# Kernel tuning notes

Measured on AMD Instinct MI355X. Metric: run time of the kernel, lower is better.

The kernel has to match this reference:

```python
import jax, jax.numpy as jnp
import numpy as np

KH = KW = 3
K = KH * KW
STRIDE = 1
PAD = 1
DIL = 1
GROUPS = 1
DG = 1  # deformable_groups
CIN = 256
COUT = 256
DC = 64  # depth_channels


def conv2d(x, w, b):
    out = jax.lax.conv_general_dilated(
        x, w, (STRIDE, STRIDE), [(PAD, PAD), (PAD, PAD)],
        rhs_dilation=(DIL, DIL), dimension_numbers=('NCHW', 'OIHW', 'NCHW'))
    return out + b[None, :, None, None]


def deform_sample(x, offset, mask):
    """Modulated deformable im2col. x:[N,C,H,W], offset:[N,DG*2*K,Ho,Wo],
    mask:[N,DG*K,Ho,Wo] or None. Returns cols [N,C,K,Ho,Wo]."""
    N, C, H, W = x.shape
    Ho = (H + 2 * PAD - (DIL * (KH - 1) + 1)) // STRIDE + 1
    Wo = (W + 2 * PAD - (DIL * (KW - 1) + 1)) // STRIDE + 1
    ky, kx = jnp.meshgrid(jnp.arange(KH), jnp.arange(KW), indexing='ij')
    # base sampling grid per kernel tap: [K,Ho,Wo]
    base_y = (jnp.arange(Ho) * STRIDE - PAD)[None, :, None] + (ky.reshape(-1) * DIL)[:, None, None]
    base_x = (jnp.arange(Wo) * STRIDE - PAD)[None, None, :] + (kx.reshape(-1) * DIL)[:, None, None]
    off = offset.reshape(N, DG, K, 2, Ho, Wo)  # [...,0]=dy, [...,1]=dx (CUDA layout)
    y = base_y[None, None].astype(x.dtype) + off[:, :, :, 0]
    xx = base_x[None, None].astype(x.dtype) + off[:, :, :, 1]
    y0 = jnp.floor(y)
    x0 = jnp.floor(xx)
    ly = y - y0
    lx = xx - x0
    y0i = y0.astype(jnp.int32)
    x0i = x0.astype(jnp.int32)
    xg = x.reshape(N, DG, C // DG, H * W)

    def gather(iy, ix):
        valid = ((iy >= 0) & (iy < H) & (ix >= 0) & (ix < W)).astype(x.dtype)
        idx = (jnp.clip(iy, 0, H - 1) * W + jnp.clip(ix, 0, W - 1)).reshape(N, DG, 1, K * Ho * Wo)
        v = jnp.take_along_axis(xg, idx, axis=3).reshape(N, DG, C // DG, K, Ho, Wo)
        return v * valid[:, :, None]

    v00 = gather(y0i, x0i)
    v01 = gather(y0i, x0i + 1)
    v10 = gather(y0i + 1, x0i)
    v11 = gather(y0i + 1, x0i + 1)
    w00 = (1 - ly) * (1 - lx)
    w01 = (1 - ly) * lx
    w10 = ly * (1 - lx)
    w11 = ly * lx
    cols = (v00 * w00[:, :, None] + v01 * w01[:, :, None]
            + v10 * w10[:, :, None] + v11 * w11[:, :, None])
    if mask is not None:
        cols = cols * mask.reshape(N, DG, 1, K, Ho, Wo)
    return cols.reshape(N, C, K, Ho, Wo)


def deform_conv2d(x, offset, mask, weight, bias):
    cols = deform_sample(x, offset, mask)  # [N,C,K,Ho,Wo]
    N, C, _, Ho, Wo = cols.shape
    Cout = weight.shape[0]
    cg = C // GROUPS
    cols = cols.reshape(N, GROUPS, cg * K, Ho * Wo)
    wg = weight.reshape(GROUPS, Cout // GROUPS, cg * K)
    out = jnp.einsum('gok,ngkp->ngop', wg, cols).reshape(N, Cout, Ho, Wo)
    return out + bias[None, :, None, None]


def setup_inputs() -> dict:
    key = jax.random.key(0)
    ks = jax.random.split(key, 8)
    x = jax.random.normal(ks[0], (4, CIN, 64, 64), dtype=jnp.float32)
    depth = jax.random.normal(ks[1], (4, DC, 64, 64), dtype=jnp.float32)
    stdv = 1.0 / np.sqrt(CIN * KH * KW)
    weight = jax.random.uniform(ks[2], (COUT, CIN // GROUPS, KH, KW), minval=-stdv, maxval=stdv, dtype=jnp.float32)
    bias = jnp.zeros((COUT,), jnp.float32)
    # offset/mask convs are zero-init in the module; use small random weights
    # so the irregular gather path is actually exercised.
    off_w = 0.05 * jax.random.normal(ks[3], (DG * 2 * K, CIN + DC, KH, KW), dtype=jnp.float32)
    off_b = 0.05 * jax.random.normal(ks[4], (DG * 2 * K,), dtype=jnp.float32)
    mask_w = 0.05 * jax.random.normal(ks[5], (DG * K, DC, KH, KW), dtype=jnp.float32)
    mask_b = 0.05 * jax.random.normal(ks[6], (DG * K,), dtype=jnp.float32)
    return {"x": x, "depth": depth, "weight": weight, "bias": bias,
            "off_w": off_w, "off_b": off_b, "mask_w": mask_w, "mask_b": mask_b}


def reference(x, depth, weight, bias, off_w, off_b, mask_w, mask_b):
    # offset = conv_offset(cat(x, depth))
    offset = conv2d(jnp.concatenate([x, depth], axis=1), off_w, off_b)
    # mask = sigmoid(DeformConv(depth, offset))  (non-modulated deform conv)
    mask = jax.nn.sigmoid(deform_conv2d(depth, offset, None, mask_w, mask_b))
    # modulated deformable conv on x
    return deform_conv2d(x, offset, mask, weight, bias)
```

## Files before the change

kernel.cpp:

```cpp
#include <hip/hip_runtime.h>


typedef __bf16 bf16x8 __attribute__((ext_vector_type(8)));
typedef float f32x4 __attribute__((ext_vector_type(4)));
typedef float float2_u __attribute__((ext_vector_type(2), aligned(4)));

__device__ __forceinline__ unsigned short f2bf(float f) {
  unsigned b = __float_as_uint(f);
  return (unsigned short)((b + 0x7fffu + ((b >> 16) & 1u)) >> 16);
}

__global__ __launch_bounds__(256) void k_prep_weight(
    const float* __restrict__ w, unsigned short* __restrict__ wbf)
{
  const int i = blockIdx.x * 256 + threadIdx.x;
  wbf[i] = f2bf(w[i]);
}

__global__ __launch_bounds__(256) void k_offset_conv(
    const float* __restrict__ x, const float* __restrict__ depth,
    const float* __restrict__ off_w, const float* __restrict__ off_b,
    float* __restrict__ offs)
{
  const int seg = blockIdx.x >> 8;
  const int nh  = blockIdx.x & 255;
  const int n = nh >> 6, ho = nh & 63;
  const int tid = threadIdx.x;
  const int lane = tid & 63;
  const int wave = tid >> 6;

  float acc[18];
#pragma unroll
  for (int i = 0; i < 18; ++i) acc[i] = 0.f;

  const int c0 = __builtin_amdgcn_readfirstlane(seg * 80 + wave * 20);

  for (int ci = 0; ci < 20; ++ci) {
    const int c = c0 + ci;
    const float* p = (c < 256) ? (x + (((n << 8) + c) << 12))
                               : (depth + (((n << 6) + (c - 256)) << 12));
    const float v0 = (ho > 0)  ? p[((ho - 1) << 6) + lane] : 0.f;
    const float v1 =             p[( ho      << 6) + lane];
    const float v2 = (ho < 63) ? p[((ho + 1) << 6) + lane] : 0.f;

    float v[9];
#pragma unroll
    for (int ky = 0; ky < 3; ++ky) {
      const float r = (ky == 0) ? v0 : ((ky == 1) ? v1 : v2);
#pragma unroll
      for (int kx = 0; kx < 3; ++kx) {
        const int src = lane + kx - 1;
        const float s = __shfl(r, src & 63);
        v[ky * 3 + kx] = (src >= 0 && src < 64) ? s : 0.f;
      }
    }
    const float* wp = off_w + c * 9;
#pragma unroll
    for (int co = 0; co < 18; ++co) {
      const float* w = wp + co * 2880;
#pragma unroll
      for (int t = 0; t < 9; ++t) acc[co] += v[t] * w[t];
    }
  }

  __shared__ float red[4][18][64];
#pragma unroll
  for (int co = 0; co < 18; ++co) red[wave][co][lane] = acc[co];
  __syncthreads();
  for (int o = tid; o < 18 * 64; o += 256) {
    const int co = o >> 6, wo = o & 63;
    float s = red[0][co][wo] + red[1][co][wo] + red[2][co][wo] + red[3][co][wo];
    if (seg == 0) s += off_b[co];
    atomicAdd(&offs[((n * 18 + co) << 12) + (ho << 6) + wo], s);
  }
}

__global__ __launch_bounds__(512) void k_mask_conv(
    const float* __restrict__ depth, const float* __restrict__ offs,
    const float* __restrict__ mask_w, const float* __restrict__ mask_b,
    float* __restrict__ mask)
{
  const int n  = blockIdx.x >> 6;
  const int ho = blockIdx.x & 63;
  const int tid  = threadIdx.x;
  const int lane = tid & 63;
  const int wave = tid >> 6;
  const int wo = lane;

  int i00[9], i01[9], i10[9], i11[9];
  float cw00[9], cw01[9], cw10[9], cw11[9];
  const float* op = offs + ((n * 18) << 12) + (ho << 6) + wo;
#pragma unroll
  for (int k = 0; k < 9; ++k) {
    const float dy = op[(2 * k) << 12];
    const float dx = op[(2 * k + 1) << 12];
    const float yy = (float)(ho - 1 + k / 3) + dy;
    const float xx = (float)(wo - 1 + k % 3) + dx;
    const float y0f = floorf(yy), x0f = floorf(xx);
    const float ly = yy - y0f, lx = xx - x0f;
    const int y0 = (int)y0f, x0 = (int)x0f;
    const int y0c = min(max(y0, 0), 63),     x0c = min(max(x0, 0), 63);
    const int y1c = min(max(y0 + 1, 0), 63), x1c = min(max(x0 + 1, 0), 63);
    const float fy0 = (y0 >= 0 && y0 < 64) ? 1.f : 0.f;
    const float fy1 = (y0 >= -1 && y0 < 63) ? 1.f : 0.f;
    const float fx0 = (x0 >= 0 && x0 < 64) ? 1.f : 0.f;
    const float fx1 = (x0 >= -1 && x0 < 63) ? 1.f : 0.f;
    i00[k] = (y0c << 6) + x0c;  i01[k] = (y0c << 6) + x1c;
    i10[k] = (y1c << 6) + x0c;  i11[k] = (y1c << 6) + x1c;
    cw00[k] = (1.f - ly) * (1.f - lx) * fy0 * fx0;
    cw01[k] = (1.f - ly) * lx * fy0 * fx1;
    cw10[k] = ly * (1.f - lx) * fy1 * fx0;
    cw11[k] = ly * lx * fy1 * fx1;
  }

  float acc[9];
#pragma unroll
  for (int i = 0; i < 9; ++i) acc[i] = 0.f;

  const int cbase = __builtin_amdgcn_readfirstlane(wave * 8);
  for (int cc = 0; cc < 8; ++cc) {
    const int c = cbase + cc;
    const float* p = depth + (((n << 6) + c) << 12);
    float val[9];
#pragma unroll
    for (int k = 0; k < 9; ++k) {
      val[k] = p[i00[k]] * cw00[k] + p[i01[k]] * cw01[k] +
               p[i10[k]] * cw10[k] + p[i11[k]] * cw11[k];
    }
    const float* wp = mask_w + c * 9;
#pragma unroll
    for (int co = 0; co < 9; ++co) {
#pragma unroll
      for (int k = 0; k < 9; ++k) acc[co] += val[k] * wp[co * 576 + k];
    }
  }

  __shared__ float red[8][9][64];
#pragma unroll
  for (int co = 0; co < 9; ++co) red[wave][co][lane] = acc[co];
  __syncthreads();
  for (int o = tid; o < 9 * 64; o += 512) {
    const int co = o >> 6, w2 = o & 63;
    float s = mask_b[co];
#pragma unroll
    for (int w = 0; w < 8; ++w) s += red[w][co][w2];
    mask[((n * 9 + co) << 12) + (ho << 6) + w2] = 1.f / (1.f + expf(-s));
  }
}

__global__ __launch_bounds__(512, 2) void k_deform_gemm(
    const float* __restrict__ x, const float* __restrict__ offs,
    const float* __restrict__ mask, const unsigned short* __restrict__ wbf,
    const float* __restrict__ bias, float* __restrict__ out)
{
  __shared__ __align__(16) unsigned short Bs[2][64][72];
  __shared__ float4 pwT[9][64];
  __shared__ int2   piT[9][64];

  const int tid = threadIdx.x;
  const int b    = blockIdx.x;
  const int xcd  = b & 7, slot = b >> 3;
  const int n    = xcd >> 1;
  const int ho0  = ((xcd & 1) << 5) + slot;
  const int pxb  = ho0 << 6;
  const int pxg0 = (n << 12) + pxb;

  for (int e = tid; e < 576; e += 512) {
    const int tap = e >> 6, pl = e & 63;
    const int pxg = pxg0 + pl;
    const int wo = pl;
    const float dy = offs[((n * 18 + 2 * tap) << 12) + pxb + pl];
    const float dx = offs[((n * 18 + 2 * tap + 1) << 12) + pxb + pl];
    const float m  = mask[((n * 9 + tap) << 12) + pxb + pl];
    (void)pxg;
    const float yy = (float)(ho0 - 1 + tap / 3) + dy;
    const float xx = (float)(wo - 1 + tap % 3) + dx;
    const float y0f = floorf(yy), x0f = floorf(xx);
    const float ly = yy - y0f, lx = xx - x0f;
    const int y0 = (int)y0f, x0 = (int)x0f;
    const int y0c = min(max(y0, 0), 63);
    const int y1c = min(max(y0 + 1, 0), 63);
    const float fy0 = (y0 >= 0 && y0 < 64) ? 1.f : 0.f;
    const float fy1 = (y0 >= -1 && y0 < 63) ? 1.f : 0.f;
    const int x0c = min(max(x0, 0), 63);
    const int x1c = min(max(x0 + 1, 0), 63);
    const int bx  = min(max(x0, 0), 62);
    const float vx0 = (x0 >= 0 && x0 < 64) ? 1.f : 0.f;
    const float vx1 = (x0 >= -1 && x0 < 63) ? 1.f : 0.f;
    const float wl = (1.f - lx) * vx0 * ((x0c == bx) ? 1.f : 0.f)
                   + lx * vx1 * ((x1c == bx) ? 1.f : 0.f);
    const float wr = (1.f - lx) * vx0 * ((x0c == bx + 1) ? 1.f : 0.f)
                   + lx * vx1 * ((x1c == bx + 1) ? 1.f : 0.f);
    const float a0 = (1.f - ly) * fy0 * m;
    const float a1 = ly * fy1 * m;
    pwT[tap][pl] = make_float4(wl * a0, wr * a0, wl * a1, wr * a1);
    piT[tap][pl] = make_int2((((y0c << 6) + bx) << 2), (((y1c << 6) + bx) << 2));
  }
  __syncthreads();

  const int pxl = tid & 63;
  const int oct = tid >> 6;
  const float* xn = x + ((long)(n << 8) << 12);

  auto sample = [&](int kc, int buf) {
    const int kk0 = kc + (oct << 3);
    int c = (int)(((unsigned)kk0 * 7282u) >> 16);
    int tap = kk0 - 9 * c;
    const char* p = (const char*)(xn + (c << 12));
    __align__(16) unsigned short v[8];
#pragma unroll
    for (int j = 0; j < 8; ++j) {
      const float4 w = pwT[tap][pxl];
      const int2 ii  = piT[tap][pxl];
      const float2_u pa = *(const float2_u*)(p + ii.x);
      const float2_u pb = *(const float2_u*)(p + ii.y);
      v[j] = f2bf(pa.x * w.x + pa.y * w.y + pb.x * w.z + pb.y * w.w);
      if (++tap == 9) { tap = 0; p += 16384; }
    }
    *(int4*)&Bs[buf][pxl][oct << 3] = *(const int4*)v;
  };

  f32x4 acc[2][4];
#pragma unroll
  for (int mt = 0; mt < 2; ++mt)
#pragma unroll
    for (int nt = 0; nt < 4; ++nt)
#pragma unroll
      for (int r = 0; r < 4; ++r) acc[mt][nt][r] = 0.f;

  sample(0, 0);
  __syncthreads();

  const int wv   = oct;
  const int lane = tid & 63;
  const int mrow = lane & 15;
  const int koct = lane >> 4;

  for (int ic = 0; ic < 36; ++ic) {
    const int kc = ic << 6;
    bf16x8 af[2][2];
#pragma unroll
    for (int mt = 0; mt < 2; ++mt)
#pragma unroll
      for (int ks = 0; ks < 2; ++ks) {
        const int row = (wv << 5) + (mt << 4) + mrow;
        const int col = kc + (ks << 5) + (koct << 3);
        af[mt][ks] = *(const bf16x8*)(wbf + row * 2304 + col);
      }

    if (ic + 1 < 36) sample((ic + 1) << 6, (ic + 1) & 1);

    const int buf = ic & 1;
#pragma unroll
    for (int ks = 0; ks < 2; ++ks)
#pragma unroll
      for (int nt = 0; nt < 4; ++nt) {
        const bf16x8 bfr =
            *(const bf16x8*)&Bs[buf][(nt << 4) + mrow][(ks << 5) + (koct << 3)];
        acc[0][nt] = __builtin_amdgcn_mfma_f32_16x16x32_bf16(af[0][ks], bfr,
                                                             acc[0][nt], 0, 0, 0);
        acc[1][nt] = __builtin_amdgcn_mfma_f32_16x16x32_bf16(af[1][ks], bfr,
                                                             acc[1][nt], 0, 0, 0);
      }
    __syncthreads();
  }

#pragma unroll
  for (int mt = 0; mt < 2; ++mt)
#pragma unroll
    for (int nt = 0; nt < 4; ++nt)
#pragma unroll
      for (int r = 0; r < 4; ++r) {
        const int co = (wv << 5) + (mt << 4) + ((lane >> 4) << 2) + r;
        const int pxg = pxb + (nt << 4) + (lane & 15);
        out[(((n << 8) + co) << 12) + pxg] = acc[mt][nt][r] + bias[co];
      }
}

extern "C" void kernel_launch(void* const* d_in, const int* in_sizes, int n_in,
                              void* d_out, int out_size, void* d_ws, size_t ws_size,
                              hipStream_t stream) {
  const float* x      = (const float*)d_in[0];
  const float* depth  = (const float*)d_in[1];
  const float* weight = (const float*)d_in[2];
  const float* bias   = (const float*)d_in[3];
  const float* off_w  = (const float*)d_in[4];
  const float* off_b  = (const float*)d_in[5];
  const float* mask_w = (const float*)d_in[6];
  const float* mask_b = (const float*)d_in[7];
  float* out = (float*)d_out;

  float* offs = (float*)d_ws;
  float* mask = offs + 294912;
  unsigned short* wbf = (unsigned short*)(mask + 147456);

  hipMemsetAsync(offs, 0, 294912 * sizeof(float), stream);
  k_prep_weight<<<2304, 256, 0, stream>>>(weight, wbf);
  k_offset_conv<<<1024, 256, 0, stream>>>(x, depth, off_w, off_b, offs);
  k_mask_conv<<<256, 512, 0, stream>>>(depth, offs, mask_w, mask_b, mask);
  k_deform_gemm<<<256, 512, 0, stream>>>(x, offs, mask, wbf, bias, out);
}
```

Measured before the change: 281.2 us.

## Halve deform GEMM pixel tile and split gather into issue/finish around MFMAs

The deform GEMM tile shrinks from 64 to 32 pixels per block, so 512 blocks launch instead of 256, with launch bounds raised to allow four blocks per CU. The bilinear sampling is split into an issue phase that starts the global gathers before the MFMA loop and a finish phase that blends and stores to LDS after it, hiding gather latency behind the matrix math. The aim is more parallelism across the 256 CUs and better latency hiding. The cost is that each block reuses the weight fragments over only half as many pixels, doubling weight reads, and the 4-blocks-per-CU bound may force tighter register allocation.

```diff
diff --git a/kernel.cpp b/kernel.cpp
--- a/kernel.cpp
+++ b/kernel.cpp
@@ -148,32 +148,30 @@
   }
 }
 
-__global__ __launch_bounds__(512, 2) void k_deform_gemm(
+__global__ __launch_bounds__(512, 4) void k_deform_gemm(
     const float* __restrict__ x, const float* __restrict__ offs,
     const float* __restrict__ mask, const unsigned short* __restrict__ wbf,
     const float* __restrict__ bias, float* __restrict__ out)
 {
-  __shared__ __align__(16) unsigned short Bs[2][64][72];
-  __shared__ float4 pwT[9][64];
-  __shared__ int2   piT[9][64];
+  __shared__ __align__(16) unsigned short Bs[2][32][72];
+  __shared__ float4 pwT[9][32];
+  __shared__ int2   piT[9][32];
 
   const int tid = threadIdx.x;
   const int b    = blockIdx.x;
   const int xcd  = b & 7, slot = b >> 3;
   const int n    = xcd >> 1;
-  const int ho0  = ((xcd & 1) << 5) + slot;
-  const int pxb  = ho0 << 6;
-  const int pxg0 = (n << 12) + pxb;
-
-  for (int e = tid; e < 576; e += 512) {
-    const int tap = e >> 6, pl = e & 63;
-    const int pxg = pxg0 + pl;
-    const int wo = pl;
-    const float dy = offs[((n * 18 + 2 * tap) << 12) + pxb + pl];
-    const float dx = offs[((n * 18 + 2 * tap + 1) << 12) + pxb + pl];
-    const float m  = mask[((n * 9 + tap) << 12) + pxb + pl];
-    (void)pxg;
-    const float yy = (float)(ho0 - 1 + tap / 3) + dy;
+  const int ho   = ((xcd & 1) << 5) + (slot >> 1);
+  const int wo0  = (slot & 1) << 5;
+  const int pxb  = (ho << 6) + wo0;
+
+  if (tid < 288) {
+    const int tap = tid >> 5, pl = tid & 31;
+    const int wo = wo0 + pl;
+    const float dy = offs[((n * 18 + 2 * tap) << 12) + (ho << 6) + wo];
+    const float dx = offs[((n * 18 + 2 * tap + 1) << 12) + (ho << 6) + wo];
+    const float m  = mask[((n * 9 + tap) << 12) + (ho << 6) + wo];
+    const float yy = (float)(ho - 1 + tap / 3) + dy;
     const float xx = (float)(wo - 1 + tap % 3) + dx;
     const float y0f = floorf(yy), x0f = floorf(xx);
     const float ly = yy - y0f, lx = xx - x0f;
@@ -198,43 +196,57 @@
   }
   __syncthreads();
 
-  const int pxl = tid & 63;
-  const int oct = tid >> 6;
-  const float* xn = x + ((long)(n << 8) << 12);
-
-  auto sample = [&](int kc, int buf) {
-    const int kk0 = kc + (oct << 3);
-    int c = (int)(((unsigned)kk0 * 7282u) >> 16);
-    int tap = kk0 - 9 * c;
-    const char* p = (const char*)(xn + (c << 12));
-    __align__(16) unsigned short v[8];
-#pragma unroll
-    for (int j = 0; j < 8; ++j) {
-      const float4 w = pwT[tap][pxl];
-      const int2 ii  = piT[tap][pxl];
-      const float2_u pa = *(const float2_u*)(p + ii.x);
-      const float2_u pb = *(const float2_u*)(p + ii.y);
-      v[j] = f2bf(pa.x * w.x + pa.y * w.y + pb.x * w.z + pb.y * w.w);
-      if (++tap == 9) { tap = 0; p += 16384; }
-    }
-    *(int4*)&Bs[buf][pxl][oct << 3] = *(const int4*)v;
-  };
-
-  f32x4 acc[2][4];
-#pragma unroll
-  for (int mt = 0; mt < 2; ++mt)
-#pragma unroll
-    for (int nt = 0; nt < 4; ++nt)
-#pragma unroll
-      for (int r = 0; r < 4; ++r) acc[mt][nt][r] = 0.f;
-
-  sample(0, 0);
-  __syncthreads();
-
-  const int wv   = oct;
+  const int pxl  = tid & 31;
+  const int kq   = tid >> 5;
+  const int wv   = tid >> 6;
   const int lane = tid & 63;
   const int mrow = lane & 15;
   const int koct = lane >> 4;
+  const float* xn = x + ((long)(n << 8) << 12);
+
+  float4   w_[4];
+  float2_u pa_[4], pb_[4];
+
+  auto issue = [&](int kc) {
+    const int k0 = kc + (kq << 2);
+    int c = (int)(((unsigned)k0 * 7282u) >> 16);
+    int tt = k0 - 9 * c;
+    int2 ii[4];
+    const char* pp[4];
+    const char* p = (const char*)(xn + (c << 12));
+#pragma unroll
+    for (int j = 0; j < 4; ++j) {
+      w_[j] = pwT[tt][pxl];
+      ii[j] = piT[tt][pxl];
+      pp[j] = p;
+      if (++tt == 9) { tt = 0; p += 16384; }
+    }
+#pragma unroll
+    for (int j = 0; j < 4; ++j) {
+      pa_[j] = *(const float2_u*)(pp[j] + ii[j].x);
+      pb_[j] = *(const float2_u*)(pp[j] + ii[j].y);
+    }
+  };
+  auto finish = [&](int buf) {
+    __align__(8) unsigned short v[4];
+#pragma unroll
+    for (int j = 0; j < 4; ++j)
+      v[j] = f2bf(pa_[j].x * w_[j].x + pa_[j].y * w_[j].y +
+                  pb_[j].x * w_[j].z + pb_[j].y * w_[j].w);
+    *(int2*)&Bs[buf][pxl][kq << 2] = *(const int2*)v;
+  };
+
+  f32x4 acc[2][2];
+#pragma unroll
+  for (int mt = 0; mt < 2; ++mt)
+#pragma unroll
+    for (int nt = 0; nt < 2; ++nt)
+#pragma unroll
+      for (int r = 0; r < 4; ++r) acc[mt][nt][r] = 0.f;
+
+  issue(0);
+  finish(0);
+  __syncthreads();
 
   for (int ic = 0; ic < 36; ++ic) {
     const int kc = ic << 6;
@@ -248,13 +260,13 @@
         af[mt][ks] = *(const bf16x8*)(wbf + row * 2304 + col);
       }
 
-    if (ic + 1 < 36) sample((ic + 1) << 6, (ic + 1) & 1);
+    if (ic + 1 < 36) issue((ic + 1) << 6);
 
     const int buf = ic & 1;
 #pragma unroll
     for (int ks = 0; ks < 2; ++ks)
 #pragma unroll
-      for (int nt = 0; nt < 4; ++nt) {
+      for (int nt = 0; nt < 2; ++nt) {
         const bf16x8 bfr =
             *(const bf16x8*)&Bs[buf][(nt << 4) + mrow][(ks << 5) + (koct << 3)];
         acc[0][nt] = __builtin_amdgcn_mfma_f32_16x16x32_bf16(af[0][ks], bfr,
@@ -262,13 +274,15 @@
         acc[1][nt] = __builtin_amdgcn_mfma_f32_16x16x32_bf16(af[1][ks], bfr,
                                                              acc[1][nt], 0, 0, 0);
       }
+
+    if (ic + 1 < 36) finish((ic + 1) & 1);
     __syncthreads();
   }
 
 #pragma unroll
   for (int mt = 0; mt < 2; ++mt)
 #pragma unroll
-    for (int nt = 0; nt < 4; ++nt)
+    for (int nt = 0; nt < 2; ++nt)
 #pragma unroll
       for (int r = 0; r < 4; ++r) {
         const int co = (wv << 5) + (mt << 4) + ((lane >> 4) << 2) + r;
@@ -298,5 +312,5 @@
   k_prep_weight<<<2304, 256, 0, stream>>>(weight, wbf);
   k_offset_conv<<<1024, 256, 0, stream>>>(x, depth, off_w, off_b, offs);
   k_mask_conv<<<256, 512, 0, stream>>>(depth, offs, mask_w, mask_b, mask);
-  k_deform_gemm<<<256, 512, 0, stream>>>(x, offs, mask, wbf, bias, out);
-}
+  k_deform_gemm<<<512, 512, 0, stream>>>(x, offs, mask, wbf, bias, out);
+}
```

New measurement: 301.0 us. 7.0% more time.

## Stage input row strips in LDS via async global-to-LDS loads for bilinear gather

Applied to the files above, without the earlier changes.

The deform GEMM kernel now asynchronously copies an 18-row strip of each input channel into a 9-slot LDS ring using global_load_lds, and bilinear samples read from LDS when the row falls in the strip, falling back to global memory otherwise. The B tile goes from double-buffered to single-buffered, and the gather now runs after the MFMA stage with an extra barrier, so sampling and MMA no longer overlap. Index packing is compressed to one int. The aim is to replace scattered global gathers with LDS reads, at the cost of less compute overlap, more LDS use that may lower occupancy, and a possible race on the ring slots if the async copies are not waited on before they are read.

```diff
diff --git a/kernel.cpp b/kernel.cpp
--- a/kernel.cpp
+++ b/kernel.cpp
@@ -148,32 +148,46 @@
   }
 }
 
+__device__ __forceinline__ void stage_channel(const float* src, float* dstb,
+                                              int lane) {
+  const char* s = (const char*)src + lane * 16;
+  char* d = (char*)dstb;
+#pragma unroll
+  for (int j = 0; j < 4; ++j)
+    __builtin_amdgcn_global_load_lds(
+        (const __attribute__((address_space(1))) void*)(s + j * 1024),
+        (__attribute__((address_space(3))) void*)(d + j * 1024), 16, 0, 0);
+  if (lane < 32)
+    __builtin_amdgcn_global_load_lds(
+        (const __attribute__((address_space(1))) void*)(s + 4096),
+        (__attribute__((address_space(3))) void*)(d + 4096), 16, 0, 0);
+}
+
 __global__ __launch_bounds__(512, 2) void k_deform_gemm(
     const float* __restrict__ x, const float* __restrict__ offs,
     const float* __restrict__ mask, const unsigned short* __restrict__ wbf,
     const float* __restrict__ bias, float* __restrict__ out)
 {
-  __shared__ __align__(16) unsigned short Bs[2][64][72];
+  __shared__ float strip[9 * 1152];
+  __shared__ __align__(16) unsigned short Bs[64][72];
   __shared__ float4 pwT[9][64];
-  __shared__ int2   piT[9][64];
+  __shared__ int    piT[9][64];
 
   const int tid = threadIdx.x;
   const int b    = blockIdx.x;
-  const int xcd  = b & 7, slot = b >> 3;
+  const int xcd  = b & 7, bslot = b >> 3;
   const int n    = xcd >> 1;
-  const int ho0  = ((xcd & 1) << 5) + slot;
-  const int pxb  = ho0 << 6;
-  const int pxg0 = (n << 12) + pxb;
+  const int ho   = ((xcd & 1) << 5) + bslot;
+  const int pxb  = ho << 6;
+  const int ylo  = min(max(ho - 8, 0), 46);
 
   for (int e = tid; e < 576; e += 512) {
     const int tap = e >> 6, pl = e & 63;
-    const int pxg = pxg0 + pl;
     const int wo = pl;
     const float dy = offs[((n * 18 + 2 * tap) << 12) + pxb + pl];
     const float dx = offs[((n * 18 + 2 * tap + 1) << 12) + pxb + pl];
     const float m  = mask[((n * 9 + tap) << 12) + pxb + pl];
-    (void)pxg;
-    const float yy = (float)(ho0 - 1 + tap / 3) + dy;
+    const float yy = (float)(ho - 1 + tap / 3) + dy;
     const float xx = (float)(wo - 1 + tap % 3) + dx;
     const float y0f = floorf(yy), x0f = floorf(xx);
     const float ly = yy - y0f, lx = xx - x0f;
@@ -194,75 +208,101 @@
     const float a0 = (1.f - ly) * fy0 * m;
     const float a1 = ly * fy1 * m;
     pwT[tap][pl] = make_float4(wl * a0, wr * a0, wl * a1, wr * a1);
-    piT[tap][pl] = make_int2((((y0c << 6) + bx) << 2), (((y1c << 6) + bx) << 2));
-  }
-  __syncthreads();
-
-  const int pxl = tid & 63;
-  const int oct = tid >> 6;
-  const float* xn = x + ((long)(n << 8) << 12);
-
-  auto sample = [&](int kc, int buf) {
-    const int kk0 = kc + (oct << 3);
-    int c = (int)(((unsigned)kk0 * 7282u) >> 16);
-    int tap = kk0 - 9 * c;
-    const char* p = (const char*)(xn + (c << 12));
-    __align__(16) unsigned short v[8];
-#pragma unroll
-    for (int j = 0; j < 8; ++j) {
-      const float4 w = pwT[tap][pxl];
-      const int2 ii  = piT[tap][pxl];
-      const float2_u pa = *(const float2_u*)(p + ii.x);
-      const float2_u pb = *(const float2_u*)(p + ii.y);
-      v[j] = f2bf(pa.x * w.x + pa.y * w.y + pb.x * w.z + pb.y * w.w);
-      if (++tap == 9) { tap = 0; p += 16384; }
-    }
-    *(int4*)&Bs[buf][pxl][oct << 3] = *(const int4*)v;
-  };
-
-  f32x4 acc[2][4];
-#pragma unroll
-  for (int mt = 0; mt < 2; ++mt)
-#pragma unroll
-    for (int nt = 0; nt < 4; ++nt)
-#pragma unroll
-      for (int r = 0; r < 4; ++r) acc[mt][nt][r] = 0.f;
-
-  sample(0, 0);
-  __syncthreads();
-
-  const int wv   = oct;
+    piT[tap][pl] = bx | (y0c << 6) | (y1c << 12);
+  }
+
+  const int pxl  = tid & 63;
+  const int oct  = tid >> 6;
   const int lane = tid & 63;
   const int mrow = lane & 15;
   const int koct = lane >> 4;
+  const float* xn = x + ((long)(n << 8) << 12);
+
+  stage_channel(xn + (oct << 12) + (ylo << 6), &strip[oct * 1152], lane);
+  int c_staged = 8;
+  __syncthreads();
+
+  auto gather = [&](int ic) {
+    const int k0 = (ic << 6) + (oct << 3);
+    int c   = (int)(((unsigned)k0 * 7282u) >> 16);
+    int tap = k0 - 9 * c;
+    int slt = c - 9 * (int)(((unsigned)c * 7282u) >> 16);
+    const char* pg = (const char*)xn + (c << 14);
+    int soff = slt * 1152;
+    __align__(16) unsigned short v[8];
+#pragma unroll
+    for (int j = 0; j < 8; ++j) {
+      const float4 w = pwT[tap][pxl];
+      const int pk = piT[tap][pxl];
+      const int bx = pk & 63;
+      const int ry0 = ((pk >> 6) & 63) - ylo;
+      const int ry1 = ((pk >> 12) & 63) - ylo;
+      float a0, a1, b0, b1;
+      if ((unsigned)ry0 < 18u) {
+        const float* s = &strip[soff + (ry0 << 6) + bx]; a0 = s[0]; a1 = s[1];
+      } else {
+        const float2_u t = *(const float2_u*)(pg + (((((pk >> 6) & 63) << 6) + bx) << 2));
+        a0 = t.x; a1 = t.y;
+      }
+      if ((unsigned)ry1 < 18u) {
+        const float* s = &strip[soff + (ry1 << 6) + bx]; b0 = s[0]; b1 = s[1];
+      } else {
+        const float2_u t = *(const float2_u*)(pg + (((((pk >> 12) & 63) << 6) + bx) << 2));
+        b0 = t.x; b1 = t.y;
+      }
+      v[j] = f2bf(a0 * w.x + a1 * w.y + b0 * w.z + b1 * w.w);
+      if (++tap == 9) { tap = 0; pg += 16384; if (++slt == 9) slt = 0; soff = slt * 1152; }
+    }
+    *(int4*)&Bs[pxl][oct << 3] = *(const int4*)v;
+  };
+
+  gather(0);
+  __syncthreads();
+
+  f32x4 acc[2][4];
+#pragma unroll
+  for (int mt = 0; mt < 2; ++mt)
+#pragma unroll
+    for (int nt = 0; nt < 4; ++nt)
+#pragma unroll
+      for (int r = 0; r < 4; ++r) acc[mt][nt][r] = 0.f;
 
   for (int ic = 0; ic < 36; ++ic) {
+    if (ic < 35) {
+      const int c_end = (64 * ic + 127) / 9;
+      const int cw = c_staged + oct;
+      if (cw <= c_end) {
+        const int slt = cw - 9 * (int)(((unsigned)cw * 7282u) >> 16);
+        stage_channel(xn + (cw << 12) + (ylo << 6), &strip[slt * 1152], lane);
+      }
+      c_staged = c_end + 1;
+    }
+
     const int kc = ic << 6;
     bf16x8 af[2][2];
 #pragma unroll
     for (int mt = 0; mt < 2; ++mt)
 #pragma unroll
       for (int ks = 0; ks < 2; ++ks) {
-        const int row = (wv << 5) + (mt << 4) + mrow;
+        const int row = (oct << 5) + (mt << 4) + mrow;
         const int col = kc + (ks << 5) + (koct << 3);
         af[mt][ks] = *(const bf16x8*)(wbf + row * 2304 + col);
       }
-
-    if (ic + 1 < 36) sample((ic + 1) << 6, (ic + 1) & 1);
-
-    const int buf = ic & 1;
 #pragma unroll
     for (int ks = 0; ks < 2; ++ks)
 #pragma unroll
       for (int nt = 0; nt < 4; ++nt) {
         const bf16x8 bfr =
-            *(const bf16x8*)&Bs[buf][(nt << 4) + mrow][(ks << 5) + (koct << 3)];
+            *(const bf16x8*)&Bs[(nt << 4) + mrow][(ks << 5) + (koct << 3)];
         acc[0][nt] = __builtin_amdgcn_mfma_f32_16x16x32_bf16(af[0][ks], bfr,
                                                              acc[0][nt], 0, 0, 0);
         acc[1][nt] = __builtin_amdgcn_mfma_f32_16x16x32_bf16(af[1][ks], bfr,
                                                              acc[1][nt], 0, 0, 0);
       }
+
     __syncthreads();
+    if (ic < 35) gather(ic + 1);
+    __syncthreads();
   }
 
 #pragma unroll
@@ -271,7 +311,7 @@
     for (int nt = 0; nt < 4; ++nt)
 #pragma unroll
       for (int r = 0; r < 4; ++r) {
-        const int co = (wv << 5) + (mt << 4) + ((lane >> 4) << 2) + r;
+        const int co = (oct << 5) + (mt << 4) + ((lane >> 4) << 2) + r;
         const int pxg = pxb + (nt << 4) + (lane & 15);
         out[(((n << 8) + co) << 12) + pxg] = acc[mt][nt][r] + bias[co];
       }
```

Result: slower. 303.8 us (+8.0%).
